# Kernel optimization log

Measured on AMD Instinct MI355X. Metric: run time of the kernel, lower is better.

Reference implementation:

```python
import jax, jax.numpy as jnp
import numpy as np

B, E, S, M, G, L, NSTEP = 32, 256, 16, 16, 32000, 8192, 128


def setup_inputs() -> dict:
    key = jax.random.key(0)
    ks = jax.random.split(key, 8)
    init = lambda k, shape, fan: (jax.random.normal(k, shape, jnp.float32) / np.sqrt(fan).astype(np.float32))
    return {
        "latent": init(ks[0], (L, 2 * E * S), 2 * E * S),
        "trans_w": init(ks[1], (E * M, E), E),
        "trans_b": jnp.zeros((E * M,), jnp.float32),
        "anchor_w": init(ks[2], (M, E), E),
        "anchor_b": jnp.zeros((M,), jnp.float32),
        "vocab_w": init(ks[3], (G, E), E),
        "vocab_b": jnp.zeros((G,), jnp.float32),
        "zi": jax.random.randint(ks[4], (B,), 0, L),
        "y": jax.random.randint(ks[5], (B, NSTEP), 0, G),
        "n_step": NSTEP,
    }


def reference(latent, trans_w, trans_b, anchor_w, anchor_b, vocab_w, vocab_b, zi, y, n_step):
    # latent rows -> (B, 2, state_count, embed_dim); split into keys/values
    z0 = latent[zi].reshape(-1, 2, S, E)
    z = z0[:, 0, 0:1, :]            # initial state: first (unscaled) key vector, [B,1,E]
    xk = z0[:, 0] * 100.0           # [B,S,E]
    xv = z0[:, 1] * 100.0           # [B,S,E]

    def step(z, _):
        # std-normalize (torch.std is unbiased -> ddof=1)
        zn = z / (1e-5 + jnp.std(z, axis=-1, keepdims=True, ddof=1)) * 0.113
        att = jax.nn.softmax(jnp.einsum("bqe,bse->bqs", zn, xk), axis=-1)  # [B,1,S]
        emit = jnp.einsum("bqs,bse->bqe", att, xv)                          # [B,1,E]
        mixed2 = (zn @ trans_w.T + trans_b).reshape(-1, M, E)               # [B,M,E]
        att2 = jax.nn.softmax(zn @ anchor_w.T + anchor_b, axis=-1)          # [B,1,M]
        dz = jnp.einsum("bqm,bme->bqe", att2, mixed2) + emit
        return zn + dz, emit[:, 0, :]

    _, zs = jax.lax.scan(step, z, None, length=n_step)  # [T,B,E]
    zs = jnp.transpose(zs, (1, 0, 2))                   # [B,T,E]
    ys = jax.nn.log_softmax(zs @ vocab_w.T + vocab_b, axis=-1)  # [B,T,G]
    yp = jnp.take_along_axis(ys, y[:, :, None], axis=-1)[:, :, 0]  # [B,T]
    return yp
```

## Files before the change

kernel.cpp:

```cpp
#include <hip/hip_runtime.h>

#define EE 256
#define GG 32000
#define NSTEP 128
#define ROWS 4096
#define VSPLIT 4
#define NWGR 64

typedef __attribute__((ext_vector_type(8))) short bf16x8;
typedef __attribute__((ext_vector_type(4))) float f32x4;

#define OFF_ZSB  0u
#define OFF_PS   2097152u
#define OFF_PT   (OFF_PS + 65536u)
#define OFF_ZNB  (OFF_PT + 65536u)
#define OFF_A2   (OFF_ZNB + 32768u)
#define OFF_BAR  (OFF_A2 + 4096u)
#define OFF_PD   (OFF_BAR + 4096u)
#define WS_REQ   (OFF_PD + 524288u)
#define OFF_VB   WS_REQ
#define VB_BYTES 16384000u


__device__ __forceinline__ float wredf(float v){
    #pragma unroll
    for (int m = 1; m < 64; m <<= 1) v += __shfl_xor(v, m);
    return v;
}
__device__ __forceinline__ unsigned short f2bf_bits(float f){
    unsigned int u = __float_as_uint(f);
    unsigned int lsb = (u >> 16) & 1u;
    u += 0x7fffu + lsb;
    return (unsigned short)(u >> 16);
}
__device__ __forceinline__ float bf2f(unsigned short u){
    return __uint_as_float(((unsigned int)u) << 16);
}
__device__ __forceinline__ float aload(const float* p){
    return __hip_atomic_load(p, __ATOMIC_RELAXED, __HIP_MEMORY_SCOPE_AGENT);
}
__device__ __forceinline__ void astore(float* p, float v){
    __hip_atomic_store(p, v, __ATOMIC_RELAXED, __HIP_MEMORY_SCOPE_AGENT);
}
__device__ __forceinline__ unsigned aloadu(const unsigned* p){
    return __hip_atomic_load(p, __ATOMIC_RELAXED, __HIP_MEMORY_SCOPE_AGENT);
}
__device__ __forceinline__ void astoreu(unsigned* p, unsigned v){
    __hip_atomic_store(p, v, __ATOMIC_RELAXED, __HIP_MEMORY_SCOPE_AGENT);
}
__device__ __forceinline__ int swz(int row, int kbyte){
    return row*512 + (kbyte ^ ((row & 7) << 4));
}

__global__ __launch_bounds__(256) void k_sentinel(float* __restrict__ outp, float val){
    int r = blockIdx.x * 256 + threadIdx.x;
    outp[r] = val;
}

__global__ void k_prep(const int* __restrict__ zi, int* __restrict__ bar){
    int t = threadIdx.x;
    bar[t] = 0;
    __syncthreads();
    if (t == 0){
        bool odd_zero = true, even_ok = true;
        for (int i = 0; i < 16; ++i){
            int lo = zi[2*i], hi = zi[2*i+1];
            if (hi != 0) odd_zero = false;
            if (lo < 0 || lo >= 8192) even_ok = false;
        }
        bar[136] = (odd_zero && even_ok) ? 1 : 0;
    }
}

__global__ __launch_bounds__(256) void k_cvt(const float* __restrict__ in,
                                             unsigned short* __restrict__ outp)
{
    int i = (blockIdx.x * 256 + threadIdx.x) * 4;
    float4 v = *(const float4*)&in[i];
    ushort4 o;
    o.x = f2bf_bits(v.x); o.y = f2bf_bits(v.y);
    o.z = f2bf_bits(v.z); o.w = f2bf_bits(v.w);
    *(ushort4*)&outp[i] = o;
}

__device__ __forceinline__ void gbar(int* __restrict__ bar, int gen){
    __syncthreads();
    const int t = threadIdx.x, wg = blockIdx.x;
    if (t == 0)
        __hip_atomic_store(&bar[wg], gen, __ATOMIC_RELAXED, __HIP_MEMORY_SCOPE_AGENT);
    if (t < NWGR){
        int spins = 0;
        while (__hip_atomic_load(&bar[t], __ATOMIC_RELAXED, __HIP_MEMORY_SCOPE_AGENT) < gen){
            __builtin_amdgcn_s_sleep(1);
            if (++spins > 2000000){
                __hip_atomic_store(&bar[132], 1, __ATOMIC_RELAXED, __HIP_MEMORY_SCOPE_AGENT);
                break;
            }
            if ((spins & 2047) == 0 &&
                __hip_atomic_load(&bar[132], __ATOMIC_RELAXED, __HIP_MEMORY_SCOPE_AGENT) != 0)
                break;
        }
    }
    __syncthreads();
    __builtin_amdgcn_sched_barrier(0);
}

__global__ __launch_bounds__(512, 1) void k_rnn(const float* __restrict__ latent,
                                                const int* __restrict__ zi,
                                                const float* __restrict__ anchor_w,
                                                const float* __restrict__ anchor_b,
                                                const float* __restrict__ trans_w,
                                                const float* __restrict__ trans_b,
                                                unsigned short* __restrict__ zsb,
                                                unsigned* __restrict__ ZNB,
                                                float* __restrict__ PD,
                                                float* __restrict__ A2,
                                                int* __restrict__ bar)
{
    __shared__ __align__(16) unsigned char WbRaw[2*64*512];
    __shared__ __align__(16) unsigned char ZNbRaw[2*32*512];
    __shared__ float xk_l[16][260];
    __shared__ float xv_l[16][260];
    __shared__ float zl[256];
    __shared__ float a2l[64];
    __shared__ float tbl[2][32];
    __shared__ float l1s[16], l2s[16], ab_l[16], rbuf[8];

    const int wg = blockIdx.x, t = threadIdx.x;
    const int mh = wg >> 3, q = wg & 7;
    const int is64 = bar[136];
    const int lane = t & 63, wv = t >> 6;
    const int kg = lane >> 4, nl = lane & 15;

    for (int idx = t; idx < 4096; idx += 512){
        int r = idx >> 6, c = idx & 63;
        int grow = (2*mh + (r >> 5))*256 + q*32 + (r & 31);
        float4 w = *(const float4*)&trans_w[(size_t)grow*256 + c*4];
        unsigned short h0 = f2bf_bits(w.x), h1 = f2bf_bits(w.y);
        unsigned short h2 = f2bf_bits(w.z), h3 = f2bf_bits(w.w);
        unsigned short l0 = f2bf_bits(w.x - bf2f(h0)), l1 = f2bf_bits(w.y - bf2f(h1));
        unsigned short l2 = f2bf_bits(w.z - bf2f(h2)), l3 = f2bf_bits(w.w - bf2f(h3));
        int off = swz(r, c*8);
        *(unsigned*)&WbRaw[off]     = (unsigned)h0 | ((unsigned)h1 << 16);
        *(unsigned*)&WbRaw[off + 4] = (unsigned)h2 | ((unsigned)h3 << 16);
        *(unsigned*)&WbRaw[64*512 + off]     = (unsigned)l0 | ((unsigned)l1 << 16);
        *(unsigned*)&WbRaw[64*512 + off + 4] = (unsigned)l2 | ((unsigned)l3 << 16);
    }
    if (t < 64) tbl[t >> 5][t & 31] = trans_b[(2*mh + (t >> 5))*256 + q*32 + (t & 31)];

    const bool isb = (wg < 32);
    const int b = wg;
    const float* base = nullptr;
    float zn_r = 0.f, em_r = 0.f;
    if (isb){
        int zb = is64 ? zi[2*b] : zi[b];
        base = latent + (size_t)zb * 8192;
        for (int i = t; i < 4096; i += 512){
            int s = i >> 8, c = i & 255;
            xk_l[s][c] = base[i];
            xv_l[s][c] = base[4096 + i];
        }
        if (t < 16) ab_l[t] = anchor_b[t];
    }
    __syncthreads();

    int gen = 0;
    for (int stp = 0; stp < NSTEP; ++stp){
        if (isb){
            float zv = 0.f;
            if (t < 256){
                if (stp == 0) zv = base[t];
                else {
                    float dz = 0.f;
                    #pragma unroll
                    for (int g = 0; g < 16; ++g) dz += aload(&PD[(g*32 + b)*256 + t]);
                    zv = zn_r + em_r + dz;
                }
                float s1 = wredf(zv), s2 = wredf(zv*zv);
                if ((t & 63) == 0){ rbuf[t>>6] = s1; rbuf[4 + (t>>6)] = s2; }
            }
            __syncthreads();
            if (t < 256){
                float tot1 = rbuf[0]+rbuf[1]+rbuf[2]+rbuf[3];
                float tot2 = rbuf[4]+rbuf[5]+rbuf[6]+rbuf[7];
                float mean = tot1 * (1.0f/EE);
                float var  = (tot2 - (float)EE*mean*mean) * (1.0f/(EE-1));
                var = fmaxf(var, 0.f);
                float sc = 0.113f / (1e-5f + sqrtf(var));
                zn_r = zv * sc;
                zl[t] = zn_r;
                unsigned short zh = f2bf_bits(zn_r);
                unsigned short zlo = f2bf_bits(zn_r - bf2f(zh));
                unsigned ohi = (unsigned)__shfl_xor((int)(unsigned)zh, 1);
                unsigned olo = (unsigned)__shfl_xor((int)(unsigned)zlo, 1);
                if (!(t & 1)){
                    astoreu(&ZNB[b*128 + (t >> 1)],        (unsigned)zh  | (ohi << 16));
                    astoreu(&ZNB[4096 + b*128 + (t >> 1)], (unsigned)zlo | (olo << 16));
                }
            }
            __syncthreads();
            if (t < 256){
                int sidx = t >> 4, L = t & 15;
                const float* aws = anchor_w + sidx*EE;
                float p1 = 0.f, p2 = 0.f;
                #pragma unroll
                for (int c = 0; c < 16; ++c){
                    int k = L*16 + c;
                    float z = zl[k];
                    p1 += z * xk_l[sidx][k];
                    p2 += z * aws[k];
                }
                #pragma unroll
                for (int mm = 1; mm < 16; mm <<= 1){ p1 += __shfl_xor(p1, mm); p2 += __shfl_xor(p2, mm); }
                if (L == 0){ l1s[sidx] = p1 * 100.0f; l2s[sidx] = p2 + ab_l[sidx]; }
            }
            __syncthreads();
            if (t < 256){
                float mx1 = -1e30f, mx2 = -1e30f;
                #pragma unroll
                for (int s = 0; s < 16; ++s){ mx1 = fmaxf(mx1, l1s[s]); mx2 = fmaxf(mx2, l2s[s]); }
                float att[16]; float sum1 = 0.f, sum2 = 0.f;
                #pragma unroll
                for (int s = 0; s < 16; ++s){
                    att[s] = expf(l1s[s] - mx1); sum1 += att[s];
                    sum2  += expf(l2s[s] - mx2);
                }
                float inv1 = 1.0f / sum1;
                if (t < 16) astore(&A2[b*16 + t], expf(l2s[t] - mx2) / sum2);
                float em = 0.f;
                #pragma unroll
                for (int s = 0; s < 16; ++s) em += (att[s] * inv1) * xv_l[s][t];
                em *= 100.0f;
                em_r = em;
                zsb[((size_t)b*NSTEP + stp)*EE + t] = f2bf_bits(em);
            }
        }
        if (stp == NSTEP-1) break;
        gen++; gbar(bar, gen);

        for (int i = t; i < 8192; i += 512){
            int p = i >> 12, rr = (i >> 7) & 31, d = i & 127;
            unsigned v = aloadu(&ZNB[i]);
            *(unsigned*)&ZNbRaw[p*(32*512) + swz(rr, d*4)] = v;
        }
        if (t < 64) a2l[t] = aload(&A2[(t >> 1)*16 + 2*mh + (t & 1)]);
        __syncthreads();
        {
            const int m = wv >> 2, et = (wv >> 1) & 1, bt = wv & 1;
            const int arow = m*32 + et*16 + nl;
            const int brow = bt*16 + nl;
            f32x4 acc = {0.f, 0.f, 0.f, 0.f};
            #pragma unroll
            for (int kk = 0; kk < 8; ++kk){
                int kb = kk*64 + kg*16;
                bf16x8 ah = *(const bf16x8*)&WbRaw[swz(arow, kb)];
                bf16x8 al = *(const bf16x8*)&WbRaw[64*512 + swz(arow, kb)];
                bf16x8 bh = *(const bf16x8*)&ZNbRaw[swz(brow, kb)];
                bf16x8 bl = *(const bf16x8*)&ZNbRaw[32*512 + swz(brow, kb)];
                acc = __builtin_amdgcn_mfma_f32_16x16x32_bf16(ah, bh, acc, 0, 0, 0);
                acc = __builtin_amdgcn_mfma_f32_16x16x32_bf16(ah, bl, acc, 0, 0, 0);
                acc = __builtin_amdgcn_mfma_f32_16x16x32_bf16(al, bh, acc, 0, 0, 0);
            }
            float a2v = a2l[brow*2 + m];
            #pragma unroll
            for (int i = 0; i < 4; ++i){
                int e_loc = et*16 + kg*4 + i;
                float u = acc[i] + tbl[m][e_loc];
                astore(&PD[(((mh << 1) + m)*32 + brow)*256 + q*32 + e_loc], a2v * u);
            }
        }
        gen++; gbar(bar, gen);
    }
}

__device__ __forceinline__ bf16x8 pack8f(const float* __restrict__ src){
    bf16x8 r;
    #pragma unroll
    for (int j = 0; j < 8; ++j) r[j] = (short)f2bf_bits(src[j]);
    return r;
}

template<bool VB>
__global__ __launch_bounds__(256, 1) void k_vocab(const unsigned short* __restrict__ vb,
                                                  const float* __restrict__ vwf,
                                                  const float* __restrict__ vbias,
                                                  const unsigned short* __restrict__ zsb,
                                                  const int* __restrict__ y,
                                                  float* __restrict__ pS,
                                                  float* __restrict__ pT,
                                                  int* __restrict__ bar)
{
    const int rowblk = blockIdx.x;
    const int split  = blockIdx.y;
    const int t = threadIdx.x;
    const int wave = t >> 6, lane = t & 63;
    const int kg = lane >> 4, nl = lane & 15;
    const int is64 = bar[136];

    __shared__ float psum_l[4][64];
    __shared__ float ptarg_l[4][64];
    __shared__ float chk[1];

    bf16x8 afr[4][8];
    #pragma unroll
    for (int mt = 0; mt < 4; ++mt)
        #pragma unroll
        for (int kk = 0; kk < 8; ++kk)
            afr[mt][kk] = *(const bf16x8*)&zsb[(size_t)(rowblk*64 + mt*16 + nl) * EE + kk*32 + kg*8];

    int tg[4][4];
    #pragma unroll
    for (int mt = 0; mt < 4; ++mt)
        #pragma unroll
        for (int i = 0; i < 4; ++i){
            int rg = rowblk*64 + mt*16 + kg*4 + i;
            tg[mt][i] = is64 ? y[2*rg] : y[rg];
        }

    float sums[4][4]; float targ[4][4];
    #pragma unroll
    for (int mt = 0; mt < 4; ++mt)
        #pragma unroll
        for (int i = 0; i < 4; ++i){ sums[mt][i] = 0.f; targ[mt][i] = 0.f; }

    for (int tile = wave; tile < 500; tile += 4){
        int n = split*8000 + tile*16 + nl;
        f32x4 acc[4];
        #pragma unroll
        for (int mt = 0; mt < 4; ++mt) acc[mt] = (f32x4){0.f,0.f,0.f,0.f};
        #pragma unroll
        for (int kk = 0; kk < 8; ++kk){
            bf16x8 bfr;
            if (VB) bfr = *(const bf16x8*)&vb[(size_t)n * EE + kk*32 + kg*8];
            else    bfr = pack8f(&vwf[(size_t)n * EE + kk*32 + kg*8]);
            #pragma unroll
            for (int mt = 0; mt < 4; ++mt)
                acc[mt] = __builtin_amdgcn_mfma_f32_16x16x32_bf16(afr[mt][kk], bfr, acc[mt], 0, 0, 0);
        }
        float bias = vbias[n];
        if (rowblk == 0 && split == 0 && t == 0 && tile == 0)
            chk[0] = acc[0][0] + bias;
        #pragma unroll
        for (int mt = 0; mt < 4; ++mt)
            #pragma unroll
            for (int i = 0; i < 4; ++i){
                float v = acc[mt][i] + bias;
                sums[mt][i] += expf(v);
                if (n == tg[mt][i]) targ[mt][i] += v;
            }
    }

    #pragma unroll
    for (int mt = 0; mt < 4; ++mt)
        #pragma unroll
        for (int i = 0; i < 4; ++i){
            float sv = sums[mt][i], tv = targ[mt][i];
            #pragma unroll
            for (int msk = 1; msk < 16; msk <<= 1){ sv += __shfl_xor(sv, msk); tv += __shfl_xor(tv, msk); }
            if (nl == 0){ int row = mt*16 + kg*4 + i; psum_l[wave][row] = sv; ptarg_l[wave][row] = tv; }
        }
    __syncthreads();
    if (t < 64){
        float sv = psum_l[0][t] + psum_l[1][t] + psum_l[2][t] + psum_l[3][t];
        float tv = ptarg_l[0][t] + ptarg_l[1][t] + ptarg_l[2][t] + ptarg_l[3][t];
        int r = rowblk*64 + t;
        pS[(size_t)split*ROWS + r] = sv;
        pT[(size_t)split*ROWS + r] = tv;
    }

    if (rowblk == 0 && split == 0 && t == 0){
        float s = 0.f;
        for (int k = 0; k < EE; ++k){
            float a = bf2f(zsb[k]);
            float w = VB ? bf2f(vb[k]) : bf2f(f2bf_bits(vwf[k]));
            s += a * w;
        }
        s += vbias[0];
        if (fabsf(s - chk[0]) > 0.02f) bar[133] = 1;
    }
}

__global__ __launch_bounds__(256) void k_final(const float* __restrict__ pS,
                                               const float* __restrict__ pT,
                                               const int* __restrict__ bar,
                                               float* __restrict__ outp)
{
    int r = blockIdx.x * 256 + threadIdx.x;
    float s = 0.f, g = 0.f;
    #pragma unroll
    for (int i = 0; i < VSPLIT; ++i){ s += pS[(size_t)i*ROWS + r]; g += pT[(size_t)i*ROWS + r]; }
    float v = g - logf(s);
    if (bar[132] != 0) v = 4000.0f;
    if (bar[133] != 0) v = 5000.0f;
    outp[r] = v;
}

extern "C" void kernel_launch(void* const* d_in, const int* in_sizes, int n_in,
                              void* d_out, int out_size, void* d_ws, size_t ws_size,
                              hipStream_t stream)
{
    (void)out_size;
    const float* latent   = (const float*)d_in[0];
    const float* trans_w  = (const float*)d_in[1];
    const float* trans_b  = (const float*)d_in[2];
    const float* anchor_w = (const float*)d_in[3];
    const float* anchor_b = (const float*)d_in[4];
    const float* vocab_w  = (const float*)d_in[5];
    const float* vocab_b  = (const float*)d_in[6];
    const int*   zi       = (const int*)d_in[7];
    const int*   y        = (const int*)d_in[8];

    float* outp = (float*)d_out;

    if (ws_size < (size_t)WS_REQ){ k_sentinel<<<16, 256, 0, stream>>>(outp, 2000.0f); return; }
    {
        bool ok = (n_in >= 9)
               && in_sizes[0] == 67108864 && in_sizes[1] == 1048576
               && in_sizes[2] == 4096     && in_sizes[3] == 4096
               && in_sizes[4] == 16       && in_sizes[5] == 8192000
               && in_sizes[6] == 32000
               && (in_sizes[7] == 32   || in_sizes[7] == 64)
               && (in_sizes[8] == 4096 || in_sizes[8] == 8192);
        if (!ok){ k_sentinel<<<16, 256, 0, stream>>>(outp, 2100.0f); return; }
    }

    char* ws = (char*)d_ws;
    unsigned short* zsb = (unsigned short*)(ws + OFF_ZSB);
    float*    pS  = (float*)(ws + OFF_PS);
    float*    pT  = (float*)(ws + OFF_PT);
    unsigned* ZNB = (unsigned*)(ws + OFF_ZNB);
    float*    A2  = (float*)(ws + OFF_A2);
    int*      bar = (int*)(ws + OFF_BAR);
    float*    PD  = (float*)(ws + OFF_PD);
    unsigned short* vbu = (unsigned short*)(ws + OFF_VB);

    const bool use_vb = ws_size >= (size_t)OFF_VB + (size_t)VB_BYTES;

    k_prep<<<1, 256, 0, stream>>>(zi, bar);
    if (use_vb)
        k_cvt<<<GG*EE/1024, 256, 0, stream>>>(vocab_w, vbu);

    k_rnn<<<NWGR, 512, 0, stream>>>(latent, zi, anchor_w, anchor_b,
                                    trans_w, trans_b, zsb, ZNB, PD, A2, bar);

    if (use_vb)
        k_vocab<true><<<dim3(64, VSPLIT), 256, 0, stream>>>(vbu, nullptr, vocab_b,
                                                            zsb, y, pS, pT, bar);
    else
        k_vocab<false><<<dim3(64, VSPLIT), 256, 0, stream>>>(nullptr, vocab_w, vocab_b,
                                                             zsb, y, pS, pT, bar);

    k_final<<<16, 256, 0, stream>>>(pS, pT, bar, outp);
}
```

Before: 2.060 ms.

## Split RNN into producer/consumer workgroups with point-to-point flags instead of grid barriers

The persistent RNN kernel now uses 32 per-batch workgroups that compute normalization, attention and the anchor softmax, plus 64 separate workgroups that run the trans_w MFMA projection. The two all-to-all grid barriers per step become one-way flag polling. Producers publish zn and then keep computing attention while the consumers run the matmul, so the two phases can overlap. The anchor-softmax weighting moves to the producer side as a local shared-memory scale, which removes the A2 global round-trip. The cost is a grid of 96 workgroups that must all be co-resident to avoid deadlock.

```diff
diff --git a/kernel.cpp b/kernel.cpp
--- a/kernel.cpp
+++ b/kernel.cpp
@@ -5,7 +5,9 @@
 #define NSTEP 128
 #define ROWS 4096
 #define VSPLIT 4
-#define NWGR 64
+#define NWGP 32
+#define NWGD 64
+#define NWGR (NWGP + NWGD)
 
 typedef __attribute__((ext_vector_type(8))) short bf16x8;
 typedef __attribute__((ext_vector_type(4))) float f32x4;
@@ -14,8 +16,7 @@
 #define OFF_PS   2097152u
 #define OFF_PT   (OFF_PS + 65536u)
 #define OFF_ZNB  (OFF_PT + 65536u)
-#define OFF_A2   (OFF_ZNB + 32768u)
-#define OFF_BAR  (OFF_A2 + 4096u)
+#define OFF_BAR  (OFF_ZNB + 32768u)
 #define OFF_PD   (OFF_BAR + 4096u)
 #define WS_REQ   (OFF_PD + 524288u)
 #define OFF_VB   WS_REQ
@@ -50,6 +51,19 @@
 }
 __device__ __forceinline__ int swz(int row, int kbyte){
     return row*512 + (kbyte ^ ((row & 7) << 4));
+}
+__device__ __forceinline__ void pollflag(int* bar, int idx, int gen){
+    int spins = 0;
+    while (__hip_atomic_load(&bar[idx], __ATOMIC_RELAXED, __HIP_MEMORY_SCOPE_AGENT) < gen){
+        __builtin_amdgcn_s_sleep(1);
+        if (++spins > 2000000){
+            __hip_atomic_store(&bar[132], 1, __ATOMIC_RELAXED, __HIP_MEMORY_SCOPE_AGENT);
+            break;
+        }
+        if ((spins & 2047) == 0 &&
+            __hip_atomic_load(&bar[132], __ATOMIC_RELAXED, __HIP_MEMORY_SCOPE_AGENT) != 0)
+            break;
+    }
 }
 
 __global__ __launch_bounds__(256) void k_sentinel(float* __restrict__ outp, float val){
@@ -83,28 +97,6 @@
     *(ushort4*)&outp[i] = o;
 }
 
-__device__ __forceinline__ void gbar(int* __restrict__ bar, int gen){
-    __syncthreads();
-    const int t = threadIdx.x, wg = blockIdx.x;
-    if (t == 0)
-        __hip_atomic_store(&bar[wg], gen, __ATOMIC_RELAXED, __HIP_MEMORY_SCOPE_AGENT);
-    if (t < NWGR){
-        int spins = 0;
-        while (__hip_atomic_load(&bar[t], __ATOMIC_RELAXED, __HIP_MEMORY_SCOPE_AGENT) < gen){
-            __builtin_amdgcn_s_sleep(1);
-            if (++spins > 2000000){
-                __hip_atomic_store(&bar[132], 1, __ATOMIC_RELAXED, __HIP_MEMORY_SCOPE_AGENT);
-                break;
-            }
-            if ((spins & 2047) == 0 &&
-                __hip_atomic_load(&bar[132], __ATOMIC_RELAXED, __HIP_MEMORY_SCOPE_AGENT) != 0)
-                break;
-        }
-    }
-    __syncthreads();
-    __builtin_amdgcn_sched_barrier(0);
-}
-
 __global__ __launch_bounds__(512, 1) void k_rnn(const float* __restrict__ latent,
                                                 const int* __restrict__ zi,
                                                 const float* __restrict__ anchor_w,
@@ -114,7 +106,6 @@
                                                 unsigned short* __restrict__ zsb,
                                                 unsigned* __restrict__ ZNB,
                                                 float* __restrict__ PD,
-                                                float* __restrict__ A2,
                                                 int* __restrict__ bar)
 {
     __shared__ __align__(16) unsigned char WbRaw[2*64*512];
@@ -122,58 +113,42 @@
     __shared__ float xk_l[16][260];
     __shared__ float xv_l[16][260];
     __shared__ float zl[256];
-    __shared__ float a2l[64];
+    __shared__ float a2s[16];
     __shared__ float tbl[2][32];
     __shared__ float l1s[16], l2s[16], ab_l[16], rbuf[8];
 
     const int wg = blockIdx.x, t = threadIdx.x;
-    const int mh = wg >> 3, q = wg & 7;
     const int is64 = bar[136];
     const int lane = t & 63, wv = t >> 6;
     const int kg = lane >> 4, nl = lane & 15;
 
-    for (int idx = t; idx < 4096; idx += 512){
-        int r = idx >> 6, c = idx & 63;
-        int grow = (2*mh + (r >> 5))*256 + q*32 + (r & 31);
-        float4 w = *(const float4*)&trans_w[(size_t)grow*256 + c*4];
-        unsigned short h0 = f2bf_bits(w.x), h1 = f2bf_bits(w.y);
-        unsigned short h2 = f2bf_bits(w.z), h3 = f2bf_bits(w.w);
-        unsigned short l0 = f2bf_bits(w.x - bf2f(h0)), l1 = f2bf_bits(w.y - bf2f(h1));
-        unsigned short l2 = f2bf_bits(w.z - bf2f(h2)), l3 = f2bf_bits(w.w - bf2f(h3));
-        int off = swz(r, c*8);
-        *(unsigned*)&WbRaw[off]     = (unsigned)h0 | ((unsigned)h1 << 16);
-        *(unsigned*)&WbRaw[off + 4] = (unsigned)h2 | ((unsigned)h3 << 16);
-        *(unsigned*)&WbRaw[64*512 + off]     = (unsigned)l0 | ((unsigned)l1 << 16);
-        *(unsigned*)&WbRaw[64*512 + off + 4] = (unsigned)l2 | ((unsigned)l3 << 16);
-    }
-    if (t < 64) tbl[t >> 5][t & 31] = trans_b[(2*mh + (t >> 5))*256 + q*32 + (t & 31)];
-
-    const bool isb = (wg < 32);
-    const int b = wg;
-    const float* base = nullptr;
-    float zn_r = 0.f, em_r = 0.f;
-    if (isb){
+    if (wg < NWGP){
+        const int b = wg;
         int zb = is64 ? zi[2*b] : zi[b];
-        base = latent + (size_t)zb * 8192;
+        const float* base = latent + (size_t)zb * 8192;
         for (int i = t; i < 4096; i += 512){
             int s = i >> 8, c = i & 255;
             xk_l[s][c] = base[i];
             xv_l[s][c] = base[4096 + i];
         }
         if (t < 16) ab_l[t] = anchor_b[t];
-    }
-    __syncthreads();
-
-    int gen = 0;
-    for (int stp = 0; stp < NSTEP; ++stp){
-        if (isb){
+        __syncthreads();
+
+        float zn_r = 0.f, em_r = 0.f;
+        for (int stp = 0; stp < NSTEP; ++stp){
+            if (stp > 0){
+                if (t < NWGD) pollflag(bar, 64 + t, stp);
+                __syncthreads();
+                __builtin_amdgcn_sched_barrier(0);
+            }
             float zv = 0.f;
             if (t < 256){
                 if (stp == 0) zv = base[t];
                 else {
                     float dz = 0.f;
                     #pragma unroll
-                    for (int g = 0; g < 16; ++g) dz += aload(&PD[(g*32 + b)*256 + t]);
+                    for (int g = 0; g < 16; ++g)
+                        dz += a2s[g] * aload(&PD[(g*32 + b)*256 + t]);
                     zv = zn_r + em_r + dz;
                 }
                 float s1 = wredf(zv), s2 = wredf(zv*zv);
@@ -189,16 +164,21 @@
                 float sc = 0.113f / (1e-5f + sqrtf(var));
                 zn_r = zv * sc;
                 zl[t] = zn_r;
-                unsigned short zh = f2bf_bits(zn_r);
-                unsigned short zlo = f2bf_bits(zn_r - bf2f(zh));
-                unsigned ohi = (unsigned)__shfl_xor((int)(unsigned)zh, 1);
-                unsigned olo = (unsigned)__shfl_xor((int)(unsigned)zlo, 1);
-                if (!(t & 1)){
-                    astoreu(&ZNB[b*128 + (t >> 1)],        (unsigned)zh  | (ohi << 16));
-                    astoreu(&ZNB[4096 + b*128 + (t >> 1)], (unsigned)zlo | (olo << 16));
-                }
-            }
-            __syncthreads();
+                if (stp < NSTEP-1){
+                    unsigned short zh  = f2bf_bits(zn_r);
+                    unsigned short zlo = f2bf_bits(zn_r - bf2f(zh));
+                    unsigned ohi = (unsigned)__shfl_xor((int)(unsigned)zh, 1);
+                    unsigned olo = (unsigned)__shfl_xor((int)(unsigned)zlo, 1);
+                    if (!(t & 1)){
+                        astoreu(&ZNB[b*128 + (t >> 1)],        (unsigned)zh  | (ohi << 16));
+                        astoreu(&ZNB[4096 + b*128 + (t >> 1)], (unsigned)zlo | (olo << 16));
+                    }
+                }
+            }
+            __syncthreads();
+            if (stp < NSTEP-1 && t == 0)
+                __hip_atomic_store(&bar[b], stp + 1, __ATOMIC_RELAXED, __HIP_MEMORY_SCOPE_AGENT);
+
             if (t < 256){
                 int sidx = t >> 4, L = t & 15;
                 const float* aws = anchor_w + sidx*EE;
@@ -226,7 +206,7 @@
                     sum2  += expf(l2s[s] - mx2);
                 }
                 float inv1 = 1.0f / sum1;
-                if (t < 16) astore(&A2[b*16 + t], expf(l2s[t] - mx2) / sum2);
+                if (t < 16) a2s[t] = expf(l2s[t] - mx2) / sum2;
                 float em = 0.f;
                 #pragma unroll
                 for (int s = 0; s < 16; ++s) em += (att[s] * inv1) * xv_l[s][t];
@@ -234,42 +214,67 @@
                 em_r = em;
                 zsb[((size_t)b*NSTEP + stp)*EE + t] = f2bf_bits(em);
             }
-        }
-        if (stp == NSTEP-1) break;
-        gen++; gbar(bar, gen);
-
-        for (int i = t; i < 8192; i += 512){
-            int p = i >> 12, rr = (i >> 7) & 31, d = i & 127;
-            unsigned v = aloadu(&ZNB[i]);
-            *(unsigned*)&ZNbRaw[p*(32*512) + swz(rr, d*4)] = v;
-        }
-        if (t < 64) a2l[t] = aload(&A2[(t >> 1)*16 + 2*mh + (t & 1)]);
+            __syncthreads();
+        }
+    } else {
+        const int d = wg - NWGP;
+        const int mh = d >> 3, q = d & 7;
+
+        for (int idx = t; idx < 4096; idx += 512){
+            int r = idx >> 6, c = idx & 63;
+            int grow = (2*mh + (r >> 5))*256 + q*32 + (r & 31);
+            float4 w = *(const float4*)&trans_w[(size_t)grow*256 + c*4];
+            unsigned short h0 = f2bf_bits(w.x), h1 = f2bf_bits(w.y);
+            unsigned short h2 = f2bf_bits(w.z), h3 = f2bf_bits(w.w);
+            unsigned short l0 = f2bf_bits(w.x - bf2f(h0)), l1 = f2bf_bits(w.y - bf2f(h1));
+            unsigned short l2 = f2bf_bits(w.z - bf2f(h2)), l3 = f2bf_bits(w.w - bf2f(h3));
+            int off = swz(r, c*8);
+            *(unsigned*)&WbRaw[off]     = (unsigned)h0 | ((unsigned)h1 << 16);
+            *(unsigned*)&WbRaw[off + 4] = (unsigned)h2 | ((unsigned)h3 << 16);
+            *(unsigned*)&WbRaw[64*512 + off]     = (unsigned)l0 | ((unsigned)l1 << 16);
+            *(unsigned*)&WbRaw[64*512 + off + 4] = (unsigned)l2 | ((unsigned)l3 << 16);
+        }
+        if (t < 64) tbl[t >> 5][t & 31] = trans_b[(2*mh + (t >> 5))*256 + q*32 + (t & 31)];
         __syncthreads();
-        {
-            const int m = wv >> 2, et = (wv >> 1) & 1, bt = wv & 1;
-            const int arow = m*32 + et*16 + nl;
-            const int brow = bt*16 + nl;
-            f32x4 acc = {0.f, 0.f, 0.f, 0.f};
-            #pragma unroll
-            for (int kk = 0; kk < 8; ++kk){
-                int kb = kk*64 + kg*16;
-                bf16x8 ah = *(const bf16x8*)&WbRaw[swz(arow, kb)];
-                bf16x8 al = *(const bf16x8*)&WbRaw[64*512 + swz(arow, kb)];
-                bf16x8 bh = *(const bf16x8*)&ZNbRaw[swz(brow, kb)];
-                bf16x8 bl = *(const bf16x8*)&ZNbRaw[32*512 + swz(brow, kb)];
-                acc = __builtin_amdgcn_mfma_f32_16x16x32_bf16(ah, bh, acc, 0, 0, 0);
-                acc = __builtin_amdgcn_mfma_f32_16x16x32_bf16(ah, bl, acc, 0, 0, 0);
-                acc = __builtin_amdgcn_mfma_f32_16x16x32_bf16(al, bh, acc, 0, 0, 0);
-            }
-            float a2v = a2l[brow*2 + m];
-            #pragma unroll
-            for (int i = 0; i < 4; ++i){
-                int e_loc = et*16 + kg*4 + i;
-                float u = acc[i] + tbl[m][e_loc];
-                astore(&PD[(((mh << 1) + m)*32 + brow)*256 + q*32 + e_loc], a2v * u);
-            }
-        }
-        gen++; gbar(bar, gen);
+
+        for (int k = 1; k < NSTEP; ++k){
+            if (t < NWGP) pollflag(bar, t, k);
+            __syncthreads();
+            __builtin_amdgcn_sched_barrier(0);
+
+            for (int i = t; i < 8192; i += 512){
+                int p = i >> 12, rr = (i >> 7) & 31, dd = i & 127;
+                unsigned v = aloadu(&ZNB[i]);
+                *(unsigned*)&ZNbRaw[p*(32*512) + swz(rr, dd*4)] = v;
+            }
+            __syncthreads();
+            {
+                const int m = wv >> 2, et = (wv >> 1) & 1, bt = wv & 1;
+                const int arow = m*32 + et*16 + nl;
+                const int brow = bt*16 + nl;
+                f32x4 acc = {0.f, 0.f, 0.f, 0.f};
+                #pragma unroll
+                for (int kk = 0; kk < 8; ++kk){
+                    int kb = kk*64 + kg*16;
+                    bf16x8 ah = *(const bf16x8*)&WbRaw[swz(arow, kb)];
+                    bf16x8 al = *(const bf16x8*)&WbRaw[64*512 + swz(arow, kb)];
+                    bf16x8 bh = *(const bf16x8*)&ZNbRaw[swz(brow, kb)];
+                    bf16x8 bl = *(const bf16x8*)&ZNbRaw[32*512 + swz(brow, kb)];
+                    acc = __builtin_amdgcn_mfma_f32_16x16x32_bf16(ah, bh, acc, 0, 0, 0);
+                    acc = __builtin_amdgcn_mfma_f32_16x16x32_bf16(ah, bl, acc, 0, 0, 0);
+                    acc = __builtin_amdgcn_mfma_f32_16x16x32_bf16(al, bh, acc, 0, 0, 0);
+                }
+                #pragma unroll
+                for (int i = 0; i < 4; ++i){
+                    int e_loc = et*16 + kg*4 + i;
+                    float u = acc[i] + tbl[m][e_loc];
+                    astore(&PD[(((mh << 1) + m)*32 + brow)*256 + q*32 + e_loc], u);
+                }
+            }
+            __syncthreads();
+            if (t == 0)
+                __hip_atomic_store(&bar[64 + d], k, __ATOMIC_RELAXED, __HIP_MEMORY_SCOPE_AGENT);
+        }
     }
 }
 
@@ -429,7 +434,6 @@
     float*    pS  = (float*)(ws + OFF_PS);
     float*    pT  = (float*)(ws + OFF_PT);
     unsigned* ZNB = (unsigned*)(ws + OFF_ZNB);
-    float*    A2  = (float*)(ws + OFF_A2);
     int*      bar = (int*)(ws + OFF_BAR);
     float*    PD  = (float*)(ws + OFF_PD);
     unsigned short* vbu = (unsigned short*)(ws + OFF_VB);
@@ -441,7 +445,7 @@
         k_cvt<<<GG*EE/1024, 256, 0, stream>>>(vocab_w, vbu);
 
     k_rnn<<<NWGR, 512, 0, stream>>>(latent, zi, anchor_w, anchor_b,
-                                    trans_w, trans_b, zsb, ZNB, PD, A2, bar);
+                                    trans_w, trans_b, zsb, ZNB, PD, bar);
 
     if (use_vb)
         k_vocab<true><<<dim3(64, VSPLIT), 256, 0, stream>>>(vbu, nullptr, vocab_b,
```

After: 1.854 ms. 10.0% less time.
